# Optimization experiments

Hardware: AMD Instinct MI355X
Metric: run time of the kernel (lower is better)

## Reference

```python
import jax, jax.numpy as jnp
import numpy as np

H = 128   # hidden_dim
M = 8     # mix_dim
N = 20000 # num_nodes
E = 320000

def gelu(x):
    return jax.nn.gelu(x, approximate=False)  # torch F.gelu default is exact erf

def setup_inputs() -> dict:
    key = jax.random.key(0)
    k1, k2, k3, k4 = jax.random.split(key, 4)
    X = jax.random.normal(k1, (N, H), dtype=jnp.float32)
    edge_index = jax.random.randint(k2, (2, E), 0, N, dtype=jnp.int64)
    # Linear weights, torch layout: y = x @ W.T
    W_A = jax.random.normal(k3, (H, H), dtype=jnp.float32) / np.sqrt(H)
    W_B = jax.random.normal(k4, (M, H), dtype=jnp.float32) / np.sqrt(H)
    return {"X": X, "edge_index": edge_index, "W_A": W_A, "W_B": W_B, "num_nodes": N}

def reference(X, edge_index, W_A, W_B, num_nodes):
    src, dst = edge_index[0], edge_index[1]
    X_src = X[src]                                   # (E, h) gather
    # compute_W_tar: W_B(gelu(W_A(X_src))), input_activation=False
    W_tar_edge = gelu(X_src @ W_A.T) @ W_B.T         # (E, m)
    # per-edge outer product, scatter_add over dst
    cross = jnp.einsum('eh,em->ehm', X_src, W_tar_edge)          # (E, h, m)
    agg = jax.ops.segment_sum(cross, dst, num_segments=num_nodes) # (N, h, m)
    agg = gelu(agg)
    # gather agg back to edges, contract over mix dim
    out_edge = jnp.einsum('ehm,em->eh', agg[dst], W_tar_edge)     # (E, h)
    # scatter_mean over dst
    ones = jnp.ones((dst.shape[0],), dtype=X.dtype)
    count = jax.ops.segment_sum(ones, dst, num_segments=num_nodes)
    out_sum = jax.ops.segment_sum(out_edge, dst, num_segments=num_nodes)
    out = out_sum / jnp.maximum(count, 1.0)[:, None]
    return out
```

## Files before the change

kernel.cpp:

```cpp
#include <hip/hip_runtime.h>


#define H 128
#define MDIM 8
#define CAP 64
#define CONV_BLOCKS 16

typedef float v2f __attribute__((ext_vector_type(2)));
typedef float f32x4 __attribute__((ext_vector_type(4)));
typedef short bf16x8 __attribute__((ext_vector_type(8)));
typedef unsigned int uint2v __attribute__((ext_vector_type(2)));

union FragCvt { unsigned int u[4]; bf16x8 s8; };

__device__ __forceinline__ void gload_lds16(const void* g, void* l) {
    __builtin_amdgcn_global_load_lds(
        (const __attribute__((address_space(1))) unsigned int*)g,
        (__attribute__((address_space(3))) unsigned int*)l, 16, 0, 0);
}

__device__ __forceinline__ float gelu_f(float x) {
    float x2 = x * x;
    float u  = x * (0.7978845608f + 0.0356774081f * x2);
    float u2 = u * u;
    float num = u * (945.0f + u2 * (105.0f + u2));
    float den = 945.0f + u2 * (420.0f + 15.0f * u2);
    float t = num * __builtin_amdgcn_rcpf(den);
    t = fminf(fmaxf(t, -1.0f), 1.0f);
    return 0.5f * (x + x * t);
}

__device__ __forceinline__ v2f gelu2(v2f x) {
    v2f x2 = x * x;
    v2f u  = x * (0.7978845608f + 0.0356774081f * x2);
    v2f u2 = u * u;
    v2f num = u * (945.0f + u2 * (105.0f + u2));
    v2f den = 945.0f + u2 * (420.0f + 15.0f * u2);
    v2f t;
    t.x = num.x * __builtin_amdgcn_rcpf(den.x);
    t.y = num.y * __builtin_amdgcn_rcpf(den.y);
    t.x = fminf(fmaxf(t.x, -1.0f), 1.0f);
    t.y = fminf(fmaxf(t.y, -1.0f), 1.0f);
    return 0.5f * (x + x * t);
}

__global__ __launch_bounds__(256) void k_fill(const float* __restrict__ WA,
                                              const int* __restrict__ ei,
                                              int* __restrict__ cnt,
                                              int* __restrict__ bucket,
                                              char* __restrict__ wsWAhl,
                                              int N, int E) {
    const int b = blockIdx.x;
    const int t = threadIdx.x;

    if (b < CONV_BLOCKS) {
        int j = b * 256 + t;
        int r = j >> 5, c4 = j & 31;
        f32x4 v = *(const f32x4*)(WA + (size_t)r * H + c4 * 4);
        unsigned int u0 = __float_as_uint(v.x);
        unsigned int u1 = __float_as_uint(v.y);
        unsigned int u2 = __float_as_uint(v.z);
        unsigned int u3 = __float_as_uint(v.w);
        float l0 = v.x - __uint_as_float(u0 & 0xFFFF0000u);
        float l1 = v.y - __uint_as_float(u1 & 0xFFFF0000u);
        float l2 = v.z - __uint_as_float(u2 & 0xFFFF0000u);
        float l3 = v.w - __uint_as_float(u3 & 0xFFFF0000u);
        uint2v hh, ll;
        hh.x = (u0 >> 16) | (u1 & 0xFFFF0000u);
        hh.y = (u2 >> 16) | (u3 & 0xFFFF0000u);
        ll.x = (__float_as_uint(l0) >> 16) | (__float_as_uint(l1) & 0xFFFF0000u);
        ll.y = (__float_as_uint(l2) >> 16) | (__float_as_uint(l3) & 0xFFFF0000u);
        int off = r * 256 + ((c4 * 8) ^ ((r & 7) << 4));
        *(uint2v*)(wsWAhl + off)         = hh;
        *(uint2v*)(wsWAhl + 32768 + off) = ll;
    }

    const int stride = gridDim.x * 256;
    const int e0 = b * 256 + t;
    const int e1 = e0 + stride;
    const bool v1 = (e1 < E);
    int s0 = ei[e0];
    int d0 = ei[E + e0];
    int s1 = v1 ? ei[e1] : 0;
    int d1 = v1 ? ei[E + e1] : 0;
    int p0 = atomicAdd(&cnt[d0], 1);
    int p1 = v1 ? atomicAdd(&cnt[d1], 1) : CAP;
    if (p0 < CAP) bucket[d0 * CAP + p0] = s0;
    if (v1 && p1 < CAP) bucket[d1 * CAP + p1] = s1;
}

__global__ __launch_bounds__(128) void k_prep(const float* __restrict__ X,
                                              const float* __restrict__ WB,
                                              const char* __restrict__ wsWAhl,
                                              float* __restrict__ T, int N) {
    __shared__ __align__(16) char lds[65536];
    char* WAh = lds;
    char* WAl = lds + 32768;

    const int t    = threadIdx.x;
    const int n0   = blockIdx.x * 32;
    const int w    = t >> 6;
    const int lane = t & 63;
    const int tj   = lane & 15;
    const int tc   = lane >> 4;

    const float* xp = X + (size_t)(n0 + w * 16 + tj) * H + tc * 8;
    f32x4 xr[8];
    #pragma unroll
    for (int ks = 0; ks < 4; ++ks) {
        xr[2 * ks]     = *(const f32x4*)(xp + ks * 32);
        xr[2 * ks + 1] = *(const f32x4*)(xp + ks * 32 + 4);
    }

    #pragma unroll
    for (int i = 0; i < 32; ++i) {
        int c = w * 32 + i;
        gload_lds16(wsWAhl + c * 1024 + lane * 16, lds + c * 1024);
    }
    __syncthreads();

    f32x4 acc[8] = {};
    #pragma unroll
    for (int ks = 0; ks < 4; ++ks) {
        f32x4 a0 = xr[2 * ks], a1 = xr[2 * ks + 1];
        unsigned int u0 = __float_as_uint(a0.x), u1 = __float_as_uint(a0.y);
        unsigned int u2 = __float_as_uint(a0.z), u3 = __float_as_uint(a0.w);
        unsigned int u4 = __float_as_uint(a1.x), u5 = __float_as_uint(a1.y);
        unsigned int u6 = __float_as_uint(a1.z), u7 = __float_as_uint(a1.w);
        FragCvt ch, cl;
        ch.u[0] = (u0 >> 16) | (u1 & 0xFFFF0000u);
        ch.u[1] = (u2 >> 16) | (u3 & 0xFFFF0000u);
        ch.u[2] = (u4 >> 16) | (u5 & 0xFFFF0000u);
        ch.u[3] = (u6 >> 16) | (u7 & 0xFFFF0000u);
        float m0 = a0.x - __uint_as_float(u0 & 0xFFFF0000u);
        float m1 = a0.y - __uint_as_float(u1 & 0xFFFF0000u);
        float m2 = a0.z - __uint_as_float(u2 & 0xFFFF0000u);
        float m3 = a0.w - __uint_as_float(u3 & 0xFFFF0000u);
        float m4 = a1.x - __uint_as_float(u4 & 0xFFFF0000u);
        float m5 = a1.y - __uint_as_float(u5 & 0xFFFF0000u);
        float m6 = a1.z - __uint_as_float(u6 & 0xFFFF0000u);
        float m7 = a1.w - __uint_as_float(u7 & 0xFFFF0000u);
        cl.u[0] = (__float_as_uint(m0) >> 16) | (__float_as_uint(m1) & 0xFFFF0000u);
        cl.u[1] = (__float_as_uint(m2) >> 16) | (__float_as_uint(m3) & 0xFFFF0000u);
        cl.u[2] = (__float_as_uint(m4) >> 16) | (__float_as_uint(m5) & 0xFFFF0000u);
        cl.u[3] = (__float_as_uint(m6) >> 16) | (__float_as_uint(m7) & 0xFFFF0000u);
        bf16x8 ah = ch.s8, al = cl.s8;

        int woff = ((ks * 64 + tc * 16) ^ ((tj & 7) << 4));
        #pragma unroll
        for (int ct = 0; ct < 8; ++ct) {
            int rb = (ct * 16 + tj) * 256;
            bf16x8 bh = *(const bf16x8*)(WAh + rb + woff);
            bf16x8 bl = *(const bf16x8*)(WAl + rb + woff);
            acc[ct] = __builtin_amdgcn_mfma_f32_16x16x32_bf16(ah, bh, acc[ct], 0, 0, 0);
            acc[ct] = __builtin_amdgcn_mfma_f32_16x16x32_bf16(al, bh, acc[ct], 0, 0, 0);
            acc[ct] = __builtin_amdgcn_mfma_f32_16x16x32_bf16(ah, bl, acc[ct], 0, 0, 0);
        }
    }
    __syncthreads();

    float (*Hs)[132]  = (float(*)[132])lds;
    float (*WBs)[132] = (float(*)[132])(lds + 32768);
    #pragma unroll
    for (int i = 0; i < 2; ++i) {
        int idx = t + 128 * i;
        int r = idx >> 5, c4 = idx & 31;
        *(f32x4*)&WBs[r][c4 * 4] = *(const f32x4*)(WB + (size_t)r * H + c4 * 4);
    }
    #pragma unroll
    for (int ct = 0; ct < 8; ++ct)
        #pragma unroll
        for (int q = 0; q < 4; ++q)
            Hs[w * 16 + tc * 4 + q][ct * 16 + tj] = gelu_f(acc[ct][q]);
    __syncthreads();

    #pragma unroll
    for (int i = 0; i < 2; ++i) {
        int q = t + 128 * i;
        int n = q >> 3, m = q & 7;
        float s = 0.f;
        #pragma unroll 4
        for (int kk = 0; kk < 32; ++kk) {
            float4 h = *(const float4*)&Hs[n][kk * 4];
            float4 wv = *(const float4*)&WBs[m][kk * 4];
            s += h.x * wv.x + h.y * wv.y + h.z * wv.z + h.w * wv.w;
        }
        T[(size_t)(n0 + n) * MDIM + m] = s;
    }
}

__device__ __forceinline__ void fma8v(v2f* acc, v2f xv, float4 ta, float4 tb) {
    acc[0] += xv * ta.x;
    acc[1] += xv * ta.y;
    acc[2] += xv * ta.z;
    acc[3] += xv * ta.w;
    acc[4] += xv * tb.x;
    acc[5] += xv * tb.y;
    acc[6] += xv * tb.z;
    acc[7] += xv * tb.w;
}

__global__ __launch_bounds__(256) void k_main(const float* __restrict__ X,
                                              const float* __restrict__ T,
                                              const int* __restrict__ cnt,
                                              const int* __restrict__ bucket,
                                              float* __restrict__ out, int N) {
    __shared__ __attribute__((aligned(16))) int srcs[4][CAP];
    __shared__ float Tl[4][CAP][MDIM];
    const int w    = threadIdx.x >> 6;
    const int lane = threadIdx.x & 63;
    const int d    = blockIdx.x * 4 + w;
    if (d >= N) return;

    const int c   = cnt[d];
    int     s_raw = bucket[d * CAP + lane];
    const int cc  = (c < CAP) ? c : CAP;
    int s = s_raw;
    s = (s < 0) ? 0 : s;
    s = (s >= N) ? 0 : s;
    srcs[w][lane] = s;
    if (lane < cc) {
        const float4* t4 = (const float4*)(T + (size_t)s * MDIM);
        *(float4*)&Tl[w][lane][0] = t4[0];
        *(float4*)&Tl[w][lane][4] = t4[1];
    }

    float sp = 0.f;
    {
        const int m = lane & 7, g = lane >> 3;
        for (int j = g; j < cc; j += 8) sp += Tl[w][j][m];
        sp += __shfl_xor(sp, 8);
        sp += __shfl_xor(sp, 16);
        sp += __shfl_xor(sp, 32);
    }
    float S[MDIM];
    #pragma unroll
    for (int m = 0; m < MDIM; ++m) S[m] = __shfl(sp, m);

    v2f acc[MDIM] = {};
    const float* Xl = X + 2 * lane;

    int j = 0;
    for (; j + 8 <= cc; j += 8) {
        int4 sa = *(const int4*)&srcs[w][j];
        int4 sb = *(const int4*)&srcs[w][j + 4];
        v2f x0 = *(const v2f*)(Xl + (size_t)sa.x * H);
        v2f x1 = *(const v2f*)(Xl + (size_t)sa.y * H);
        v2f x2 = *(const v2f*)(Xl + (size_t)sa.z * H);
        v2f x3 = *(const v2f*)(Xl + (size_t)sa.w * H);
        v2f x4 = *(const v2f*)(Xl + (size_t)sb.x * H);
        v2f x5 = *(const v2f*)(Xl + (size_t)sb.y * H);
        v2f x6 = *(const v2f*)(Xl + (size_t)sb.z * H);
        v2f x7 = *(const v2f*)(Xl + (size_t)sb.w * H);
        #pragma unroll
        for (int q = 0; q < 8; ++q) {
            float4 ta = *(const float4*)&Tl[w][j + q][0];
            float4 tb = *(const float4*)&Tl[w][j + q][4];
            v2f xv = (q == 0) ? x0 : (q == 1) ? x1 : (q == 2) ? x2 : (q == 3) ? x3
                   : (q == 4) ? x4 : (q == 5) ? x5 : (q == 6) ? x6 : x7;
            fma8v(acc, xv, ta, tb);
        }
    }
    for (; j + 4 <= cc; j += 4) {
        int4 s4 = *(const int4*)&srcs[w][j];
        v2f x0 = *(const v2f*)(Xl + (size_t)s4.x * H);
        v2f x1 = *(const v2f*)(Xl + (size_t)s4.y * H);
        v2f x2 = *(const v2f*)(Xl + (size_t)s4.z * H);
        v2f x3 = *(const v2f*)(Xl + (size_t)s4.w * H);
        fma8v(acc, x0, *(const float4*)&Tl[w][j + 0][0], *(const float4*)&Tl[w][j + 0][4]);
        fma8v(acc, x1, *(const float4*)&Tl[w][j + 1][0], *(const float4*)&Tl[w][j + 1][4]);
        fma8v(acc, x2, *(const float4*)&Tl[w][j + 2][0], *(const float4*)&Tl[w][j + 2][4]);
        fma8v(acc, x3, *(const float4*)&Tl[w][j + 3][0], *(const float4*)&Tl[w][j + 3][4]);
    }
    for (; j < cc; ++j) {
        int ss = srcs[w][j];
        v2f xv = *(const v2f*)(Xl + (size_t)ss * H);
        float4 ta = *(const float4*)&Tl[w][j][0];
        float4 tb = *(const float4*)&Tl[w][j][4];
        fma8v(acc, xv, ta, tb);
    }

    v2f r = {0.f, 0.f};
    if (c > 0) {
        float inv = __builtin_amdgcn_rcpf((float)c);
        #pragma unroll
        for (int m = 0; m < MDIM; ++m) r += gelu2(acc[m]) * S[m];
        r.x *= inv;
        r.y *= inv;
    }
    *(v2f*)(out + (size_t)d * H + 2 * lane) = r;
}

extern "C" void kernel_launch(void* const* d_in, const int* in_sizes, int n_in,
                              void* d_out, int out_size, void* d_ws, size_t ws_size,
                              hipStream_t stream) {
    const float* X  = (const float*)d_in[0];
    const int*   ei = (const int*)d_in[1];
    const float* WA = (const float*)d_in[2];
    const float* WB = (const float*)d_in[3];
    float* out = (float*)d_out;

    const int N = in_sizes[0] / H;
    const int E = in_sizes[1] / 2;

    char* wp = (char*)d_ws;
    float* T      = (float*)wp;  wp += (size_t)N * MDIM * sizeof(float);
    int*   cnt    = (int*)wp;    wp += (size_t)((N + 3) & ~3) * sizeof(int);
    int*   bucket = (int*)wp;    wp += (size_t)N * CAP * sizeof(int);
    char*  wsWAhl = wp;

    hipMemsetAsync(cnt, 0, (size_t)N * sizeof(int), stream);
    k_fill<<<dim3(641), dim3(256), 0, stream>>>(WA, ei, cnt, bucket, wsWAhl, N, E);
    k_prep<<<dim3(N / 32), dim3(128), 0, stream>>>(X, WB, wsWAhl, T, N);
    k_main<<<dim3((N + 3) / 4), dim3(256), 0, stream>>>(X, T, cnt, bucket, out, N);
}
```

Before: 127.6 us.

## Replace global-atomic bucket fill with LDS histogram, scan, and deterministic scatter

Builds the per-destination edge buckets with per-block shared-memory histograms (packed 16-bit counters), a column scan over block histograms, and a separate scatter pass. This replaces the global atomicAdd on cnt and the memset, and makes bucket order follow edge order. The main kernel also gets a double-buffered software pipeline over groups of 8 neighbor gathers, with zero-padded T rows so partial groups are handled uniformly. The cost is two extra launches, a rank array, and a serial scan over G=50 block histograms, plus the LDS histogram capping grid size at 50 blocks.

Result: slower. 142.3 us (+11.5%).

```diff
diff --git a/kernel.cpp b/kernel.cpp
--- a/kernel.cpp
+++ b/kernel.cpp
@@ -5,6 +5,7 @@
 #define MDIM 8
 #define CAP 64
 #define CONV_BLOCKS 16
+#define EPB 6400
 
 typedef float v2f __attribute__((ext_vector_type(2)));
 typedef float f32x4 __attribute__((ext_vector_type(4)));
@@ -44,17 +45,18 @@
     return 0.5f * (x + x * t);
 }
 
-__global__ __launch_bounds__(256) void k_fill(const float* __restrict__ WA,
+__global__ __launch_bounds__(256) void k_hist(const float* __restrict__ WA,
                                               const int* __restrict__ ei,
-                                              int* __restrict__ cnt,
-                                              int* __restrict__ bucket,
+                                              int* __restrict__ rank,
+                                              int* __restrict__ hist,
                                               char* __restrict__ wsWAhl,
                                               int N, int E) {
-    const int b = blockIdx.x;
+    __shared__ __align__(16) int lh[10000];
+    const int g = blockIdx.x;
     const int t = threadIdx.x;
 
-    if (b < CONV_BLOCKS) {
-        int j = b * 256 + t;
+    if (g < CONV_BLOCKS) {
+        int j = g * 256 + t;
         int r = j >> 5, c4 = j & 31;
         f32x4 v = *(const f32x4*)(WA + (size_t)r * H + c4 * 4);
         unsigned int u0 = __float_as_uint(v.x);
@@ -75,18 +77,67 @@
         *(uint2v*)(wsWAhl + 32768 + off) = ll;
     }
 
-    const int stride = gridDim.x * 256;
-    const int e0 = b * 256 + t;
-    const int e1 = e0 + stride;
-    const bool v1 = (e1 < E);
-    int s0 = ei[e0];
-    int d0 = ei[E + e0];
-    int s1 = v1 ? ei[e1] : 0;
-    int d1 = v1 ? ei[E + e1] : 0;
-    int p0 = atomicAdd(&cnt[d0], 1);
-    int p1 = v1 ? atomicAdd(&cnt[d1], 1) : CAP;
-    if (p0 < CAP) bucket[d0 * CAP + p0] = s0;
-    if (v1 && p1 < CAP) bucket[d1 * CAP + p1] = s1;
+    const int NW = N >> 1;
+    int4 z4 = {0, 0, 0, 0};
+    #pragma unroll
+    for (int i = 0; i < 10; ++i) {
+        int idx = t + 256 * i;
+        if (idx < (NW >> 2)) ((int4*)lh)[idx] = z4;
+    }
+    __syncthreads();
+
+    const int base = g * EPB;
+    #pragma unroll 1
+    for (int i = 0; i < EPB / 256; ++i) {
+        int e = base + t + 256 * i;
+        if (e < E) {
+            int d   = ei[E + e];
+            int sh  = (d & 1) << 4;
+            int old = atomicAdd(&lh[d >> 1], 1 << sh);
+            rank[e] = (old >> sh) & 0xFFFF;
+        }
+    }
+    __syncthreads();
+
+    int4* hp = (int4*)(hist + (size_t)g * NW);
+    #pragma unroll
+    for (int i = 0; i < 10; ++i) {
+        int idx = t + 256 * i;
+        if (idx < (NW >> 2)) hp[idx] = ((const int4*)lh)[idx];
+    }
+}
+
+__global__ __launch_bounds__(64) void k_scan(int* __restrict__ hist,
+                                             int* __restrict__ cnt,
+                                             int N, int G) {
+    const int NW = N >> 1;
+    int wd = blockIdx.x * 64 + threadIdx.x;
+    if (wd >= NW) return;
+    int run0 = 0, run1 = 0;
+    for (int g = 0; g < G; ++g) {
+        int v = hist[(size_t)g * NW + wd];
+        hist[(size_t)g * NW + wd] = run0 | (run1 << 16);
+        run0 += v & 0xFFFF;
+        run1 += (v >> 16) & 0xFFFF;
+    }
+    *(int2*)(cnt + 2 * wd) = make_int2(run0, run1);
+}
+
+__global__ __launch_bounds__(256) void k_scatter(const int* __restrict__ ei,
+                                                 const int* __restrict__ rank,
+                                                 const int* __restrict__ hist,
+                                                 int* __restrict__ bucket,
+                                                 int N, int E) {
+    const int NW = N >> 1;
+    int e = blockIdx.x * 256 + threadIdx.x;
+    if (e >= E) return;
+    int g = e / EPB;
+    int s = ei[e];
+    int d = ei[E + e];
+    int r = rank[e];
+    int w = hist[(size_t)g * NW + (d >> 1)];
+    int p = ((w >> ((d & 1) << 4)) & 0xFFFF) + r;
+    if (p < CAP) bucket[d * CAP + p] = s;
 }
 
 __global__ __launch_bounds__(128) void k_prep(const float* __restrict__ X,
@@ -223,6 +274,10 @@
         const float4* t4 = (const float4*)(T + (size_t)s * MDIM);
         *(float4*)&Tl[w][lane][0] = t4[0];
         *(float4*)&Tl[w][lane][4] = t4[1];
+    } else {
+        float4 z = {0.f, 0.f, 0.f, 0.f};
+        *(float4*)&Tl[w][lane][0] = z;
+        *(float4*)&Tl[w][lane][4] = z;
     }
 
     float sp = 0.f;
@@ -239,45 +294,39 @@
 
     v2f acc[MDIM] = {};
     const float* Xl = X + 2 * lane;
-
-    int j = 0;
-    for (; j + 8 <= cc; j += 8) {
-        int4 sa = *(const int4*)&srcs[w][j];
-        int4 sb = *(const int4*)&srcs[w][j + 4];
-        v2f x0 = *(const v2f*)(Xl + (size_t)sa.x * H);
-        v2f x1 = *(const v2f*)(Xl + (size_t)sa.y * H);
-        v2f x2 = *(const v2f*)(Xl + (size_t)sa.z * H);
-        v2f x3 = *(const v2f*)(Xl + (size_t)sa.w * H);
-        v2f x4 = *(const v2f*)(Xl + (size_t)sb.x * H);
-        v2f x5 = *(const v2f*)(Xl + (size_t)sb.y * H);
-        v2f x6 = *(const v2f*)(Xl + (size_t)sb.z * H);
-        v2f x7 = *(const v2f*)(Xl + (size_t)sb.w * H);
+    const int nb = (cc + 7) >> 3;
+
+    v2f xa[8], xb[8];
+    auto LB = [&](v2f* xq, int b) {
+        int4 sa = *(const int4*)&srcs[w][8 * b];
+        int4 sb = *(const int4*)&srcs[w][8 * b + 4];
+        xq[0] = *(const v2f*)(Xl + (size_t)sa.x * H);
+        xq[1] = *(const v2f*)(Xl + (size_t)sa.y * H);
+        xq[2] = *(const v2f*)(Xl + (size_t)sa.z * H);
+        xq[3] = *(const v2f*)(Xl + (size_t)sa.w * H);
+        xq[4] = *(const v2f*)(Xl + (size_t)sb.x * H);
+        xq[5] = *(const v2f*)(Xl + (size_t)sb.y * H);
+        xq[6] = *(const v2f*)(Xl + (size_t)sb.z * H);
+        xq[7] = *(const v2f*)(Xl + (size_t)sb.w * H);
+    };
+    auto FB = [&](const v2f* xq, int b) {
         #pragma unroll
-        for (int q = 0; q < 8; ++q) {
-            float4 ta = *(const float4*)&Tl[w][j + q][0];
-            float4 tb = *(const float4*)&Tl[w][j + q][4];
-            v2f xv = (q == 0) ? x0 : (q == 1) ? x1 : (q == 2) ? x2 : (q == 3) ? x3
-                   : (q == 4) ? x4 : (q == 5) ? x5 : (q == 6) ? x6 : x7;
-            fma8v(acc, xv, ta, tb);
+        for (int q = 0; q < 8; ++q)
+            fma8v(acc, xq[q], *(const float4*)&Tl[w][8 * b + q][0],
+                              *(const float4*)&Tl[w][8 * b + q][4]);
+    };
+
+    if (nb > 0) {
+        LB(xa, 0);
+        int b = 0;
+        while (true) {
+            if (b + 1 < nb) LB(xb, b + 1);
+            FB(xa, b);
+            if (++b >= nb) break;
+            if (b + 1 < nb) LB(xa, b + 1);
+            FB(xb, b);
+            if (++b >= nb) break;
         }
-    }
-    for (; j + 4 <= cc; j += 4) {
-        int4 s4 = *(const int4*)&srcs[w][j];
-        v2f x0 = *(const v2f*)(Xl + (size_t)s4.x * H);
-        v2f x1 = *(const v2f*)(Xl + (size_t)s4.y * H);
-        v2f x2 = *(const v2f*)(Xl + (size_t)s4.z * H);
-        v2f x3 = *(const v2f*)(Xl + (size_t)s4.w * H);
-        fma8v(acc, x0, *(const float4*)&Tl[w][j + 0][0], *(const float4*)&Tl[w][j + 0][4]);
-        fma8v(acc, x1, *(const float4*)&Tl[w][j + 1][0], *(const float4*)&Tl[w][j + 1][4]);
-        fma8v(acc, x2, *(const float4*)&Tl[w][j + 2][0], *(const float4*)&Tl[w][j + 2][4]);
-        fma8v(acc, x3, *(const float4*)&Tl[w][j + 3][0], *(const float4*)&Tl[w][j + 3][4]);
-    }
-    for (; j < cc; ++j) {
-        int ss = srcs[w][j];
-        v2f xv = *(const v2f*)(Xl + (size_t)ss * H);
-        float4 ta = *(const float4*)&Tl[w][j][0];
-        float4 tb = *(const float4*)&Tl[w][j][4];
-        fma8v(acc, xv, ta, tb);
     }
 
     v2f r = {0.f, 0.f};
@@ -302,15 +351,19 @@
 
     const int N = in_sizes[0] / H;
     const int E = in_sizes[1] / 2;
+    const int G = (E + EPB - 1) / EPB;
 
     char* wp = (char*)d_ws;
     float* T      = (float*)wp;  wp += (size_t)N * MDIM * sizeof(float);
     int*   cnt    = (int*)wp;    wp += (size_t)((N + 3) & ~3) * sizeof(int);
     int*   bucket = (int*)wp;    wp += (size_t)N * CAP * sizeof(int);
-    char*  wsWAhl = wp;
-
-    hipMemsetAsync(cnt, 0, (size_t)N * sizeof(int), stream);
-    k_fill<<<dim3(641), dim3(256), 0, stream>>>(WA, ei, cnt, bucket, wsWAhl, N, E);
+    char*  wsWAhl = wp;          wp += 65536;
+    int*   rank   = (int*)wp;    wp += (size_t)E * sizeof(int);
+    int*   hist   = (int*)wp;
+
+    k_hist<<<dim3(G), dim3(256), 0, stream>>>(WA, ei, rank, hist, wsWAhl, N, E);
+    k_scan<<<dim3((N / 2 + 63) / 64), dim3(64), 0, stream>>>(hist, cnt, N, G);
+    k_scatter<<<dim3((E + 255) / 256), dim3(256), 0, stream>>>(ei, rank, hist, bucket, N, E);
     k_prep<<<dim3(N / 32), dim3(128), 0, stream>>>(X, WB, wsWAhl, T, N);
     k_main<<<dim3((N + 3) / 4), dim3(256), 0, stream>>>(X, T, cnt, bucket, out, N);
 }
```

## Replace global-atomic bucket fill with LDS histogram, scan, and scatter

Applied to the files above, without the earlier changes.

Swaps the per-edge global atomicAdd bucketing for a three-pass counting sort. Each block builds a packed 16-bit LDS histogram of destinations over a chunk of edges and records per-edge ranks. A column scan then turns the histograms into per-block offsets and final counts, and a scatter pass writes sources into buckets. This removes contended global atomics and the memset, but adds two more launches and extra global traffic for rank and hist. It also hardcodes an LDS size and the bit packing that only suits N≤20000 and per-node counts under 65536.

After: 135.7 us. +6.3%, slower.

```diff
diff --git a/kernel.cpp b/kernel.cpp
--- a/kernel.cpp
+++ b/kernel.cpp
@@ -5,6 +5,8 @@
 #define MDIM 8
 #define CAP 64
 #define CONV_BLOCKS 16
+#define EPB 1280
+#define SCAN_BLOCKS 40
 
 typedef float v2f __attribute__((ext_vector_type(2)));
 typedef float f32x4 __attribute__((ext_vector_type(4)));
@@ -44,17 +46,54 @@
     return 0.5f * (x + x * t);
 }
 
-__global__ __launch_bounds__(256) void k_fill(const float* __restrict__ WA,
-                                              const int* __restrict__ ei,
+__global__ __launch_bounds__(256) void k_hist(const int* __restrict__ ei,
+                                              int* __restrict__ rank,
+                                              int* __restrict__ hist,
+                                              int N, int E) {
+    __shared__ __align__(16) int lh[10000];
+    const int g = blockIdx.x;
+    const int t = threadIdx.x;
+    const int NW = N >> 1;
+
+    int4 z4 = {0, 0, 0, 0};
+    #pragma unroll
+    for (int i = 0; i < 10; ++i) {
+        int idx = t + 256 * i;
+        if (idx < (NW >> 2)) ((int4*)lh)[idx] = z4;
+    }
+    __syncthreads();
+
+    const int base = g * EPB;
+    #pragma unroll
+    for (int i = 0; i < EPB / 256; ++i) {
+        int e = base + t + 256 * i;
+        if (e < E) {
+            int d   = ei[E + e];
+            int sh  = (d & 1) << 4;
+            int old = atomicAdd(&lh[d >> 1], 1 << sh);
+            rank[e] = (old >> sh) & 0xFFFF;
+        }
+    }
+    __syncthreads();
+
+    int4* hp = (int4*)(hist + (size_t)g * NW);
+    #pragma unroll
+    for (int i = 0; i < 10; ++i) {
+        int idx = t + 256 * i;
+        if (idx < (NW >> 2)) hp[idx] = ((const int4*)lh)[idx];
+    }
+}
+
+__global__ __launch_bounds__(256) void k_scan(int* __restrict__ hist,
                                               int* __restrict__ cnt,
-                                              int* __restrict__ bucket,
+                                              const float* __restrict__ WA,
                                               char* __restrict__ wsWAhl,
-                                              int N, int E) {
+                                              int N, int G) {
     const int b = blockIdx.x;
     const int t = threadIdx.x;
 
-    if (b < CONV_BLOCKS) {
-        int j = b * 256 + t;
+    if (b >= SCAN_BLOCKS) {
+        int j = (b - SCAN_BLOCKS) * 256 + t;
         int r = j >> 5, c4 = j & 31;
         f32x4 v = *(const f32x4*)(WA + (size_t)r * H + c4 * 4);
         unsigned int u0 = __float_as_uint(v.x);
@@ -73,20 +112,50 @@
         int off = r * 256 + ((c4 * 8) ^ ((r & 7) << 4));
         *(uint2v*)(wsWAhl + off)         = hh;
         *(uint2v*)(wsWAhl + 32768 + off) = ll;
-    }
-
-    const int stride = gridDim.x * 256;
-    const int e0 = b * 256 + t;
-    const int e1 = e0 + stride;
-    const bool v1 = (e1 < E);
-    int s0 = ei[e0];
-    int d0 = ei[E + e0];
-    int s1 = v1 ? ei[e1] : 0;
-    int d1 = v1 ? ei[E + e1] : 0;
-    int p0 = atomicAdd(&cnt[d0], 1);
-    int p1 = v1 ? atomicAdd(&cnt[d1], 1) : CAP;
-    if (p0 < CAP) bucket[d0 * CAP + p0] = s0;
-    if (v1 && p1 < CAP) bucket[d1 * CAP + p1] = s1;
+        return;
+    }
+
+    const int NW = N >> 1;
+    const int wd = b * 256 + t;
+    if (wd >= NW) return;
+    int run0 = 0, run1 = 0;
+    int gb = 0;
+    for (; gb + 8 <= G; gb += 8) {
+        int v[8];
+        #pragma unroll
+        for (int i = 0; i < 8; ++i) v[i] = hist[(size_t)(gb + i) * NW + wd];
+        #pragma unroll
+        for (int i = 0; i < 8; ++i) {
+            hist[(size_t)(gb + i) * NW + wd] = run0 | (run1 << 16);
+            run0 += v[i] & 0xFFFF;
+            run1 += (v[i] >> 16) & 0xFFFF;
+        }
+    }
+    for (; gb < G; ++gb) {
+        int v = hist[(size_t)gb * NW + wd];
+        hist[(size_t)gb * NW + wd] = run0 | (run1 << 16);
+        run0 += v & 0xFFFF;
+        run1 += (v >> 16) & 0xFFFF;
+    }
+    int2 c2; c2.x = run0; c2.y = run1;
+    *(int2*)(cnt + 2 * wd) = c2;
+}
+
+__global__ __launch_bounds__(256) void k_scatter(const int* __restrict__ ei,
+                                                 const int* __restrict__ rank,
+                                                 const int* __restrict__ hist,
+                                                 int* __restrict__ bucket,
+                                                 int N, int E) {
+    const int NW = N >> 1;
+    int e = blockIdx.x * 256 + threadIdx.x;
+    if (e >= E) return;
+    int g = e / EPB;
+    int s = ei[e];
+    int d = ei[E + e];
+    int r = rank[e];
+    int w = hist[(size_t)g * NW + (d >> 1)];
+    int p = ((w >> ((d & 1) << 4)) & 0xFFFF) + r;
+    if (p < CAP) bucket[d * CAP + p] = s;
 }
 
 __global__ __launch_bounds__(128) void k_prep(const float* __restrict__ X,
@@ -302,15 +371,21 @@
 
     const int N = in_sizes[0] / H;
     const int E = in_sizes[1] / 2;
+    const int G = (E + EPB - 1) / EPB;
 
     char* wp = (char*)d_ws;
     float* T      = (float*)wp;  wp += (size_t)N * MDIM * sizeof(float);
     int*   cnt    = (int*)wp;    wp += (size_t)((N + 3) & ~3) * sizeof(int);
     int*   bucket = (int*)wp;    wp += (size_t)N * CAP * sizeof(int);
-    char*  wsWAhl = wp;
-
-    hipMemsetAsync(cnt, 0, (size_t)N * sizeof(int), stream);
-    k_fill<<<dim3(641), dim3(256), 0, stream>>>(WA, ei, cnt, bucket, wsWAhl, N, E);
+    char*  wsWAhl = wp;          wp += 65536;
+    int*   rank   = (int*)wp;    wp += (size_t)E * sizeof(int);
+    int*   hist   = (int*)wp;
+
+    k_hist<<<dim3(G), dim3(256), 0, stream>>>(ei, rank, hist, N, E);
+    k_scan<<<dim3(SCAN_BLOCKS + CONV_BLOCKS), dim3(256), 0, stream>>>(
+        hist, cnt, WA, wsWAhl, N, G);
+    k_scatter<<<dim3((E + 255) / 256), dim3(256), 0, stream>>>(
+        ei, rank, hist, bucket, N, E);
     k_prep<<<dim3(N / 32), dim3(128), 0, stream>>>(X, WB, wsWAhl, T, N);
     k_main<<<dim3((N + 3) / 4), dim3(256), 0, stream>>>(X, T, cnt, bucket, out, N);
 }
```
